# Optimization experiments

Hardware: AMD Instinct MI355X
Metric: run time of the kernel (lower is better)

The kernel has to match this reference:

```python
import jax, jax.numpy as jnp
import numpy as np

HEAD = 64            # RWKV_HEAD_SIZE
C = 1024             # n_embd = dim_att
F = 4096             # dim_ffn
B, T = 8, 256
H = C // HEAD
N_LAYER, LAYER_ID = 12, 1
GN_EPS = 1e-5 * 8 ** 2   # GroupNorm eps = 1e-5 * head_size_divisor^2


def bshift(x):
    """bidirectional_shift_multihead: per head, first half of channels shifted
    forward in time (right), second half shifted backward (left), zero-padded."""
    b, t, c = x.shape
    x4 = x.reshape(b, t, c // HEAD, HEAD)
    mid = HEAD // 2
    f = jnp.pad(x4[:, :-1, :, :mid], ((0, 0), (1, 0), (0, 0), (0, 0)))
    r = jnp.pad(x4[:, 1:, :, mid:], ((0, 0), (0, 1), (0, 0), (0, 0)))
    return jnp.concatenate([f, r], -1).reshape(b, t, c)


def layernorm(x, g, b):
    m = jnp.mean(x, -1, keepdims=True)
    v = jnp.mean((x - m) ** 2, -1, keepdims=True)
    return (x - m) * jax.lax.rsqrt(v + 1e-5) * g + b


def groupnorm(x, g, b):
    bb, t, c = x.shape
    xg = x.reshape(bb, t, H, HEAD)
    m = jnp.mean(xg, -1, keepdims=True)
    v = jnp.mean((xg - m) ** 2, -1, keepdims=True)
    return ((xg - m) * jax.lax.rsqrt(v + GN_EPS)).reshape(bb, t, c) * g + b


def wkv6_bi(r, k, v, w, u):
    """Bidirectional WKV6. r,k,v,w: [B,T,H,N]; u: [H,N].
    y_t = r_t . (S^fwd_t + u*k_t v_t^T + S^bwd_t), with per-channel decay
    d_t = exp(-exp(w_t)) applied to the state after each step in each direction."""
    d = jnp.exp(-jnp.exp(w))
    rT, kT, vT, dT = (jnp.moveaxis(a, 1, 0) for a in (r, k, v, d))  # [T,B,H,N]
    S0 = jnp.zeros((B, H, HEAD, HEAD), r.dtype)
    uB = u[None]  # [1,H,N]

    def fstep(S, inp):
        rt, kt, vt, dt = inp
        kv = kt[..., None] * vt[..., None, :]              # [B,H,N,N]
        y = jnp.einsum('bhj,bhji->bhi', rt, S + uB[..., None] * kv)
        return dt[..., None] * S + kv, y

    _, yf = jax.lax.scan(fstep, S0, (rT, kT, vT, dT))

    def bstep(S, inp):
        rt, kt, vt, dt = inp
        y = jnp.einsum('bhj,bhji->bhi', rt, S)
        return dt[..., None] * S + kt[..., None] * vt[..., None, :], y

    _, yb = jax.lax.scan(bstep, S0, (rT, kT, vT, dT), reverse=True)
    return jnp.moveaxis(yf + yb, 0, 1)  # [B,T,H,N]


def block_forward(x, ln1_g, ln1_b, ln2_g, ln2_b,
                  maa_x, maa_w, maa_k, maa_v, maa_r, maa_g, maa_w1, maa_w2,
                  time_decay, tdw1, tdw2, u, Wr, Wk, Wv, Wg, Wo, lnx_g, lnx_b,
                  cmaa_k, cmaa_r, Wck, Wcv, Wcr):
    # ---- RWKV_Tmix_V6 (attention) branch ----
    xa = layernorm(x, ln1_g, ln1_b)
    xx = bshift(xa) - xa
    a = jnp.tanh((xa + xx * maa_x) @ maa_w1).reshape(B, T, 5, -1)   # [B,T,5,32]
    m = jnp.einsum('btfd,fdc->fbtc', a, maa_w2)                      # [5,B,T,C]
    xw = xa + xx * (maa_w + m[0])
    xk = xa + xx * (maa_k + m[1])
    xv = xa + xx * (maa_v + m[2])
    xr = xa + xx * (maa_r + m[3])
    xg = xa + xx * (maa_g + m[4])
    r = (xr @ Wr).reshape(B, T, H, HEAD)
    k = (xk @ Wk).reshape(B, T, H, HEAD)
    v = (xv @ Wv).reshape(B, T, H, HEAD)
    g = jax.nn.silu(xg @ Wg)
    w = (time_decay + jnp.tanh(xw @ tdw1) @ tdw2).reshape(B, T, H, HEAD)
    y = wkv6_bi(r, k, v, w, u).reshape(B, T, C)
    y = groupnorm(y, lnx_g, lnx_b)
    x = x + (y * g) @ Wo
    # ---- RWKV_CMix_V6 (FFN) branch ----
    xc = layernorm(x, ln2_g, ln2_b)
    cxx = bshift(xc) - xc
    kk = jnp.square(jax.nn.relu((xc + cxx * cmaa_k) @ Wck))
    kv = kk @ Wcv
    x = x + jax.nn.sigmoid((xc + cxx * cmaa_r) @ Wcr) * kv
    return x


def setup_inputs() -> dict:
    key = jax.random.key(0)
    ks = jax.random.split(key, 16)
    r1 = 1.0 - LAYER_ID / N_LAYER            # ratio_1_to_almost0
    r0 = LAYER_ID / (N_LAYER - 1)            # ratio_0_to_1
    ddd = np.arange(C, dtype=np.float64) / C
    base = (1.0 - ddd ** r1).astype(np.float32)
    half = (1.0 - ddd ** (0.5 * r1)).astype(np.float32)
    s = 0.02
    p = {}
    p['x'] = jax.random.normal(ks[0], (B, T, C), jnp.float32)
    p['ln1_g'] = jnp.ones((C,), jnp.float32)
    p['ln1_b'] = jnp.zeros((C,), jnp.float32)
    p['ln2_g'] = jnp.ones((C,), jnp.float32)
    p['ln2_b'] = jnp.zeros((C,), jnp.float32)
    p['maa_x'] = jnp.asarray(base)
    p['maa_w'] = jnp.asarray(base)
    p['maa_k'] = jnp.asarray(base)
    p['maa_v'] = jnp.asarray((1.0 - (ddd ** r1 + 0.3 * r0)).astype(np.float32))
    p['maa_r'] = jnp.asarray(half)
    p['maa_g'] = jnp.asarray(half)
    p['maa_w1'] = jax.random.uniform(ks[1], (C, 160), jnp.float32, -0.01, 0.01)
    p['maa_w2'] = jax.random.uniform(ks[2], (5, 32, C), jnp.float32, -0.01, 0.01)
    n = np.arange(C, dtype=np.float64)
    p['time_decay'] = jnp.asarray((-6.0 + 5.0 * (n / (C - 1)) ** (0.7 + 1.3 * r0)).astype(np.float32))
    p['tdw1'] = jax.random.uniform(ks[3], (C, 64), jnp.float32, -0.01, 0.01)
    p['tdw2'] = jax.random.uniform(ks[4], (64, C), jnp.float32, -0.01, 0.01)
    faaaa = r0 * (1.0 - n / (C - 1)) + ((n + 1) % 3 - 1) * 0.1
    p['u'] = jnp.asarray(faaaa.reshape(H, HEAD).astype(np.float32))
    p['Wr'] = jax.random.normal(ks[5], (C, C), jnp.float32) * s
    p['Wk'] = jax.random.normal(ks[6], (C, C), jnp.float32) * s
    p['Wv'] = jax.random.normal(ks[7], (C, C), jnp.float32) * s
    p['Wg'] = jax.random.normal(ks[8], (C, C), jnp.float32) * s
    p['Wo'] = jax.random.normal(ks[9], (C, C), jnp.float32) * s
    p['lnx_g'] = jnp.ones((C,), jnp.float32)
    p['lnx_b'] = jnp.zeros((C,), jnp.float32)
    p['cmaa_k'] = jnp.asarray(base)
    p['cmaa_r'] = jnp.asarray(base)
    p['Wck'] = jax.random.normal(ks[10], (C, F), jnp.float32) * s
    p['Wcv'] = jax.random.normal(ks[11], (F, C), jnp.float32) * s
    p['Wcr'] = jax.random.normal(ks[12], (C, C), jnp.float32) * s
    return p


def reference(x, ln1_g, ln1_b, ln2_g, ln2_b,
              maa_x, maa_w, maa_k, maa_v, maa_r, maa_g, maa_w1, maa_w2,
              time_decay, tdw1, tdw2, u, Wr, Wk, Wv, Wg, Wo, lnx_g, lnx_b,
              cmaa_k, cmaa_r, Wck, Wcv, Wcr):
    return block_forward(x, ln1_g, ln1_b, ln2_g, ln2_b,
                         maa_x, maa_w, maa_k, maa_v, maa_r, maa_g, maa_w1, maa_w2,
                         time_decay, tdw1, tdw2, u, Wr, Wk, Wv, Wg, Wo, lnx_g, lnx_b,
                         cmaa_k, cmaa_r, Wck, Wcv, Wcr)
```

## Files before the change

kernel.cpp:

```cpp
#include <hip/hip_runtime.h>
#include <math.h>
#include <stdint.h>

static constexpr int B  = 8;
static constexpr int T  = 256;
static constexpr int C  = 1024;
static constexpr int H  = 16;
static constexpr int HEAD = 64;
static constexpr int FF = 4096;
static constexpr int BT = B * T;
static constexpr int NCH = 8;
static constexpr int CS  = 32;

typedef short short8  __attribute__((ext_vector_type(8)));
typedef float floatx4 __attribute__((ext_vector_type(4)));

__device__ __forceinline__ float bf2f(ushort u) {
    return __uint_as_float(((uint32_t)u) << 16);
}
__device__ __forceinline__ ushort f2bf(float x) {
    uint32_t u = __float_as_uint(x);
    u += 0x7fff + ((u >> 16) & 1);
    return (ushort)(u >> 16);
}

__device__ __forceinline__ void gload16(const void* g, void* l) {
    __builtin_amdgcn_global_load_lds(
        (const __attribute__((address_space(1))) unsigned int*)g,
        (__attribute__((address_space(3))) unsigned int*)l, 16, 0, 0);
}

#define BEPI_NONE_BF   0
#define BEPI_SILU_BF   1
#define BEPI_RELUSQ_BF 2
#define BEPI_NONE_F    3
#define BEPI_RES_F     4
#define BEPI_SIGRES_F  5
#define BEPI_TANH_F    6
#define BEPI_TANH_BF   7
#define BEPI_DECAY_F   8
#define BEPI_SIGRES2_F 9

__global__ __launch_bounds__(256) void ln_kernel(const float* __restrict__ x,
                                                 const float* __restrict__ g,
                                                 const float* __restrict__ b,
                                                 float* __restrict__ out)
{
    const int row = blockIdx.x;
    const int tid = threadIdx.x;
    const float4 v = reinterpret_cast<const float4*>(x + (size_t)row * C)[tid];
    float s = v.x + v.y + v.z + v.w;
#pragma unroll
    for (int off = 32; off > 0; off >>= 1) s += __shfl_xor(s, off);
    __shared__ float red[8];
    const int wave = tid >> 6, lane = tid & 63;
    if (lane == 0) red[wave] = s;
    __syncthreads();
    const float mean = (red[0] + red[1] + red[2] + red[3]) * (1.0f / C);
    const float d0 = v.x - mean, d1 = v.y - mean, d2 = v.z - mean, d3 = v.w - mean;
    float q = d0 * d0 + d1 * d1 + d2 * d2 + d3 * d3;
#pragma unroll
    for (int off = 32; off > 0; off >>= 1) q += __shfl_xor(q, off);
    if (lane == 0) red[4 + wave] = q;
    __syncthreads();
    const float var = (red[4] + red[5] + red[6] + red[7]) * (1.0f / C);
    const float rstd = rsqrtf(var + 1e-5f);
    const int c = tid * 4;
    float4 o;
    o.x = d0 * rstd * g[c + 0] + b[c + 0];
    o.y = d1 * rstd * g[c + 1] + b[c + 1];
    o.z = d2 * rstd * g[c + 2] + b[c + 2];
    o.w = d3 * rstd * g[c + 3] + b[c + 3];
    reinterpret_cast<float4*>(out + (size_t)row * C)[tid] = o;
}

__global__ __launch_bounds__(256) void bshiftmix_kernel(const float* __restrict__ xa,
                                                        const float* __restrict__ maa,
                                                        float* __restrict__ xx,
                                                        ushort* __restrict__ ax)
{
    const int i = blockIdx.x * 256 + threadIdx.x;
    const int c = i & (C - 1);
    const int bt = i >> 10;
    const int t = bt & (T - 1);
    const int j = c & (HEAD - 1);
    float src = 0.f;
    if (j < HEAD / 2) { if (t > 0)     src = xa[i - C]; }
    else              { if (t < T - 1) src = xa[i + C]; }
    const float a = xa[i];
    const float xv = src - a;
    xx[i] = xv;
    ax[i] = f2bf(a + xv * maa[c]);
}

__global__ __launch_bounds__(256) void bshiftcmix_kernel(const float* __restrict__ xc,
                                                         const float* __restrict__ mk,
                                                         const float* __restrict__ mr,
                                                         ushort* __restrict__ ok,
                                                         ushort* __restrict__ orr)
{
    const int i = blockIdx.x * 256 + threadIdx.x;
    const int c = i & (C - 1);
    const int bt = i >> 10;
    const int t = bt & (T - 1);
    const int j = c & (HEAD - 1);
    float src = 0.f;
    if (j < HEAD / 2) { if (t > 0)     src = xc[i - C]; }
    else              { if (t < T - 1) src = xc[i + C]; }
    const float a = xc[i];
    const float cxx = src - a;
    ok[i]  = f2bf(a + cxx * mk[c]);
    orr[i] = f2bf(a + cxx * mr[c]);
}

__global__ __launch_bounds__(1024) void gnmul_kernel(const float* __restrict__ yf,
                                                     const float* __restrict__ yb,
                                                     const float* __restrict__ g,
                                                     const float* __restrict__ b,
                                                     const ushort* __restrict__ gate,
                                                     const ushort* __restrict__ vin,
                                                     const ushort* __restrict__ rbuf,
                                                     const ushort* __restrict__ kbuf,
                                                     const float* __restrict__ u,
                                                     ushort* __restrict__ out)
{
    const int row = blockIdx.x;
    const int tid = threadIdx.x;
    const size_t idx = (size_t)row * C + tid;
    float p = bf2f(rbuf[idx]) * bf2f(kbuf[idx]) * u[tid];
#pragma unroll
    for (int off = 32; off > 0; off >>= 1) p += __shfl_xor(p, off);
    const float v = yf[idx] + yb[idx] + p * bf2f(vin[idx]);
    float s = v;
#pragma unroll
    for (int off = 32; off > 0; off >>= 1) s += __shfl_xor(s, off);
    const float m = s * (1.0f / HEAD);
    const float d = v - m;
    float q = d * d;
#pragma unroll
    for (int off = 32; off > 0; off >>= 1) q += __shfl_xor(q, off);
    const float rstd = rsqrtf(q * (1.0f / HEAD) + 6.4e-4f);
    out[idx] = f2bf((d * rstd * g[tid] + b[tid]) * bf2f(gate[idx]));
}

__global__ __launch_bounds__(256) void wconv_kernel(const float* __restrict__ W,
                                                    ushort* __restrict__ Wt,
                                                    int Kd, int Nd)
{
    __shared__ float tile[32][33];
    const int n0 = blockIdx.x * 32, k0 = blockIdx.y * 32;
    const int tx = threadIdx.x, ty = threadIdx.y;
#pragma unroll
    for (int i = 0; i < 4; ++i)
        tile[ty * 4 + i][tx] = W[(size_t)(k0 + ty * 4 + i) * Nd + n0 + tx];
    __syncthreads();
#pragma unroll
    for (int i = 0; i < 4; ++i)
        Wt[(size_t)(n0 + ty * 4 + i) * Kd + k0 + tx] = f2bf(tile[tx][ty * 4 + i]);
}

__global__ __launch_bounds__(256) void w2conv_kernel(const float* __restrict__ w2,
                                                     ushort* __restrict__ w2t)
{
    __shared__ float tile[32][33];
    const int f = blockIdx.y;
    const int n0 = blockIdx.x * 32;
    const int tx = threadIdx.x, ty = threadIdx.y;
#pragma unroll
    for (int i = 0; i < 4; ++i)
        tile[ty * 4 + i][tx] = w2[(size_t)f * 32 * C + (size_t)(ty * 4 + i) * C + n0 + tx];
    __syncthreads();
#pragma unroll
    for (int i = 0; i < 4; ++i)
        w2t[(size_t)f * C * 32 + (size_t)(n0 + ty * 4 + i) * 32 + tx] = f2bf(tile[tx][ty * 4 + i]);
}

struct Wconv4Args { const float* W[4]; };
__global__ __launch_bounds__(256) void wconv4_kernel(Wconv4Args args, ushort* __restrict__ Wt)
{
    __shared__ float tile[32][33];
    const int z = blockIdx.z;
    const float* __restrict__ W = args.W[z];
    ushort* __restrict__ dst = Wt + (size_t)z * C * C;
    const int n0 = blockIdx.x * 32, k0 = blockIdx.y * 32;
    const int tx = threadIdx.x, ty = threadIdx.y;
#pragma unroll
    for (int i = 0; i < 4; ++i)
        tile[ty * 4 + i][tx] = W[(size_t)(k0 + ty * 4 + i) * C + n0 + tx];
    __syncthreads();
#pragma unroll
    for (int i = 0; i < 4; ++i)
        dst[(size_t)(n0 + ty * 4 + i) * C + k0 + tx] = f2bf(tile[tx][ty * 4 + i]);
}

struct Mix5Args { const float* maa[5]; ushort* out[5]; };
__global__ __launch_bounds__(256) void mix5m_kernel(const ushort* __restrict__ a5b,
                                                    const ushort* __restrict__ w2t,
                                                    const float* __restrict__ xa,
                                                    const float* __restrict__ xx,
                                                    Mix5Args args)
{
    __shared__ __align__(16) ushort As[128 * 32];
    __shared__ __align__(16) ushort Bs[64 * 32];
    const int f = blockIdx.z;
    const int bm = blockIdx.y * 128, bn = blockIdx.x * 64;
    const int tid = threadIdx.x;
    const int wid = tid >> 6, lane = tid & 63;
    const int wr = wid >> 1, wc = wid & 1;
    const int l15 = lane & 15, lhi = lane >> 4;

#pragma unroll
    for (int p = 0; p < 2; ++p) {
        const int lin = p * 256 + tid;
        const int row = lin >> 2;
        const int sp = (lin & 3) ^ ((row >> 1) & 3);
        gload16(a5b + (size_t)(bm + row) * 160 + f * 32 + sp * 8, &As[lin * 8]);
    }
    {
        const int lin = tid;
        const int n = lin >> 2;
        const int sp = (lin & 3) ^ ((n >> 1) & 3);
        gload16(w2t + ((size_t)f * C + bn + n) * 32 + sp * 8, &Bs[lin * 8]);
    }
    __syncthreads();

    short8 af[4], bfr[2];
#pragma unroll
    for (int m = 0; m < 4; ++m) {
        const int row = wr * 64 + m * 16 + l15;
        const int sp = lhi ^ ((row >> 1) & 3);
        af[m] = *(const short8*)&As[row * 32 + sp * 8];
    }
#pragma unroll
    for (int n = 0; n < 2; ++n) {
        const int col = wc * 32 + n * 16 + l15;
        const int sp = lhi ^ ((col >> 1) & 3);
        bfr[n] = *(const short8*)&Bs[col * 32 + sp * 8];
    }
    floatx4 acc[4][2];
#pragma unroll
    for (int m = 0; m < 4; ++m)
#pragma unroll
        for (int n = 0; n < 2; ++n)
            acc[m][n] = __builtin_amdgcn_mfma_f32_16x16x32_bf16(
                af[m], bfr[n], (floatx4){0.f, 0.f, 0.f, 0.f}, 0, 0, 0);

    const float* __restrict__ maa = args.maa[f];
    ushort* __restrict__ out = args.out[f];
#pragma unroll
    for (int m = 0; m < 4; ++m) {
        const int row0 = bm + wr * 64 + m * 16 + lhi * 4;
#pragma unroll
        for (int n = 0; n < 2; ++n) {
            const int col = bn + wc * 32 + n * 16 + l15;
            const float mc = maa[col];
#pragma unroll
            for (int j = 0; j < 4; ++j) {
                const size_t oi = (size_t)(row0 + j) * C + col;
                out[oi] = f2bf(xa[oi] + xx[oi] * (mc + acc[m][n][j]));
            }
        }
    }
}

__global__ __launch_bounds__(256) void wkv_pass1(const ushort* __restrict__ k,
                                                 const ushort* __restrict__ v,
                                                 const float* __restrict__ d,
                                                 ushort* __restrict__ M,
                                                 float* __restrict__ D)
{
    const int uc = blockIdx.x;
    const int w = threadIdx.x >> 6, lane = threadIdx.x & 63;
    const int c = uc & (NCH - 1), unit = uc >> 3;
    const int dir = unit & 1, bh = unit >> 1;
    const int jb = w * 16;
    const size_t rowb = ((size_t)(bh >> 4) * T * H + (bh & 15)) * HEAD;
    __shared__ float Lk[4][CS][16], Ld[4][CS][16];

    const int s0 = c * CS;
    for (int idx = lane; idx < CS * 16; idx += 64) {
        const int s = idx >> 4, jj = idx & 15;
        const int t = dir ? (T - 1 - (s0 + s)) : (s0 + s);
        const size_t g = rowb + (size_t)t * (H * HEAD) + jb + jj;
        Lk[w][s][jj] = bf2f(k[g]);
        Ld[w][s][jj] = d[g];
    }
    float vr[CS];
#pragma unroll
    for (int s = 0; s < CS; ++s) {
        const int t = dir ? (T - 1 - (s0 + s)) : (s0 + s);
        vr[s] = bf2f(v[rowb + (size_t)t * (H * HEAD) + lane]);
    }
    __syncthreads();

    float S[16];
#pragma unroll
    for (int j = 0; j < 16; ++j) S[j] = 0.f;

    for (int ss = 0; ss < CS; ++ss) {
        const float vv = vr[ss];
        const float* __restrict__ sk = Lk[w][ss];
        const float* __restrict__ sd = Ld[w][ss];
#pragma unroll
        for (int jj = 0; jj < 16; jj += 4) {
            const float4 k4 = *reinterpret_cast<const float4*>(&sk[jj]);
            const float4 d4 = *reinterpret_cast<const float4*>(&sd[jj]);
            S[jj + 0] = fmaf(d4.x, S[jj + 0], k4.x * vv);
            S[jj + 1] = fmaf(d4.y, S[jj + 1], k4.y * vv);
            S[jj + 2] = fmaf(d4.z, S[jj + 2], k4.z * vv);
            S[jj + 3] = fmaf(d4.w, S[jj + 3], k4.w * vv);
        }
    }
    const size_t mb = (size_t)uc * 4096 + (size_t)lane * 64 + jb;
#pragma unroll
    for (int j = 0; j < 16; ++j) M[mb + j] = f2bf(S[j]);
    if (lane < 16) {
        float PD = 1.f;
#pragma unroll
        for (int s = 0; s < CS; ++s) PD *= Ld[w][s][lane];
        D[(size_t)uc * 64 + jb + lane] = PD;
    }
}

__global__ __launch_bounds__(1024) void wkv_pass2(ushort* __restrict__ M,
                                                  const float* __restrict__ D)
{
    const int unit = blockIdx.x;
    const int tid = threadIdx.x;
    const int j0 = (tid & 15) * 4;
    float S0 = 0.f, S1 = 0.f, S2 = 0.f, S3 = 0.f;
#pragma unroll
    for (int c = 0; c < NCH; ++c) {
        const int uc = unit * NCH + c;
        const float4 Dv = *reinterpret_cast<const float4*>(D + (size_t)uc * 64 + j0);
        ushort* mp = M + (size_t)uc * 4096 + tid * 4;
        const uint2 mv = *reinterpret_cast<const uint2*>(mp);
        const float m0 = bf2f((ushort)(mv.x & 0xffff));
        const float m1 = bf2f((ushort)(mv.x >> 16));
        const float m2 = bf2f((ushort)(mv.y & 0xffff));
        const float m3 = bf2f((ushort)(mv.y >> 16));
        uint2 sv;
        sv.x = (uint32_t)f2bf(S0) | ((uint32_t)f2bf(S1) << 16);
        sv.y = (uint32_t)f2bf(S2) | ((uint32_t)f2bf(S3) << 16);
        *reinterpret_cast<uint2*>(mp) = sv;
        S0 = fmaf(Dv.x, S0, m0);
        S1 = fmaf(Dv.y, S1, m1);
        S2 = fmaf(Dv.z, S2, m2);
        S3 = fmaf(Dv.w, S3, m3);
    }
}

__global__ __launch_bounds__(256) void wkv_ymfma(const ushort* __restrict__ r,
                                                 const ushort* __restrict__ k,
                                                 const ushort* __restrict__ v,
                                                 const float* __restrict__ d,
                                                 const ushort* __restrict__ Sin,
                                                 float* __restrict__ yf,
                                                 float* __restrict__ yb)
{
    const int uc = blockIdx.x;
    const int c = uc & (NCH - 1), unit = uc >> 3;
    const int dir = unit & 1, bh = unit >> 1;
    const int tid = threadIdx.x;
    const int wv = tid >> 6, lane = tid & 63;
    const int l15 = lane & 15, lhi = lane >> 4;
    const size_t rowb = ((size_t)(bh >> 4) * T * H + (bh & 15)) * HEAD;
    const int s0 = c * CS;

    __shared__ ushort rp[32][64];
    __shared__ ushort kp[32][64];
    __shared__ ushort vt[64][40];
    __shared__ ushort Pl[32][32];

    for (int idx = tid; idx < 32 * 64; idx += 256) {
        const int s = idx >> 6, j = idx & 63;
        const int t = dir ? (T - 1 - (s0 + s)) : (s0 + s);
        const size_t g = rowb + (size_t)t * (H * HEAD) + j;
        const int cs = (j >> 3) ^ (s & 7);
        rp[s][cs * 8 + (j & 7)] = r[g];
        kp[s][cs * 8 + (j & 7)] = k[g];
        vt[j][s] = v[g];
    }
    __syncthreads();

    if (tid < 64) {
        const int j = tid;
        float Q = 1.f, iQ = 1.f;
        for (int s = 0; s < 32; ++s) {
            const int t = dir ? (T - 1 - (s0 + s)) : (s0 + s);
            const float dd = d[rowb + (size_t)t * (H * HEAD) + j];
            const int a = ((j >> 3) ^ (s & 7)) * 8 + (j & 7);
            rp[s][a] = f2bf(bf2f(rp[s][a]) * Q);
            Q *= dd;
            iQ *= (1.0f / dd);
            kp[s][a] = f2bf(bf2f(kp[s][a]) * iQ);
        }
    }
    __syncthreads();

    const int st = wv & 1;
    const int ip = wv >> 1;

    short8 ar[2];
#pragma unroll
    for (int ks = 0; ks < 2; ++ks) {
        const int row = st * 16 + l15;
        const int ch = (ks * 4 + lhi) ^ (row & 7);
        ar[ks] = *(const short8*)&rp[row][ch * 8];
    }

    floatx4 acc[2];
#pragma unroll
    for (int n = 0; n < 2; ++n) {
        const int i = ip * 32 + n * 16 + l15;
        const ushort* sp = Sin + (size_t)uc * 4096 + (size_t)i * 64;
        const short8 b0 = *(const short8*)&sp[lhi * 8];
        const short8 b1 = *(const short8*)&sp[32 + lhi * 8];
        acc[n] = __builtin_amdgcn_mfma_f32_16x16x32_bf16(ar[0], b0, (floatx4){0.f, 0.f, 0.f, 0.f}, 0, 0, 0);
        acc[n] = __builtin_amdgcn_mfma_f32_16x16x32_bf16(ar[1], b1, acc[n], 0, 0, 0);
    }

    if (wv < 2) {
#pragma unroll
        for (int ut = 0; ut < 2; ++ut) {
            const int urow = ut * 16 + l15;
            const short8 bk0 = *(const short8*)&kp[urow][((0 + lhi) ^ (urow & 7)) * 8];
            const short8 bk1 = *(const short8*)&kp[urow][((4 + lhi) ^ (urow & 7)) * 8];
            floatx4 pa = __builtin_amdgcn_mfma_f32_16x16x32_bf16(ar[0], bk0, (floatx4){0.f, 0.f, 0.f, 0.f}, 0, 0, 0);
            pa = __builtin_amdgcn_mfma_f32_16x16x32_bf16(ar[1], bk1, pa, 0, 0, 0);
            const int sg0 = st * 16 + lhi * 4;
            const int ug = ut * 16 + l15;
#pragma unroll
            for (int jr = 0; jr < 4; ++jr) {
                const float val = (ug < sg0 + jr) ? pa[jr] : 0.f;
                Pl[sg0 + jr][ug] = f2bf(val);
            }
        }
    }
    __syncthreads();

    short8 ap;
    {
        const int row = st * 16 + l15;
        ap = *(const short8*)&Pl[row][lhi * 8];
    }
#pragma unroll
    for (int n = 0; n < 2; ++n) {
        const int i = ip * 32 + n * 16 + l15;
        const short8 bv = *(const short8*)&vt[i][lhi * 8];
        acc[n] = __builtin_amdgcn_mfma_f32_16x16x32_bf16(ap, bv, acc[n], 0, 0, 0);
    }

    float* __restrict__ yo = dir ? yb : yf;
#pragma unroll
    for (int n = 0; n < 2; ++n) {
        const int i = ip * 32 + n * 16 + l15;
#pragma unroll
        for (int jr = 0; jr < 4; ++jr) {
            const int sg = st * 16 + lhi * 4 + jr;
            const int t = dir ? (T - 1 - (s0 + sg)) : (s0 + sg);
            yo[rowb + (size_t)t * (H * HEAD) + i] = acc[n][jr];
        }
    }
}

template <int BN>
struct GemmLds {
    ushort As[2][128 * 64];
    ushort Bs[2][BN * 64];
};

template <int BN>
__device__ __forceinline__ void gemm_body(const ushort* __restrict__ A,
                                          const ushort* __restrict__ Bt,
                                          int bm, int bn, int K, int lda, int ldb,
                                          GemmLds<BN>& lds,
                                          floatx4 (&acc)[4][BN / 32])
{
    constexpr int NF = BN / 32;
    const int tid = threadIdx.x;
    const int wid = tid >> 6, lane = tid & 63;
    const int wr = wid >> 1, wc = wid & 1;
    const int l15 = lane & 15, lhi = lane >> 4;
    const int NT = K >> 6;

    auto stage = [&](int buf, int k0) {
#pragma unroll
        for (int p = 0; p < 4; ++p) {
            const int lin = p * 256 + tid;
            const int row = lin >> 3;
            const int cs = (lin & 7) ^ (row & 7);
            gload16(A + (size_t)(bm + row) * lda + k0 + cs * 8, &lds.As[buf][lin * 8]);
        }
#pragma unroll
        for (int p = 0; p < NF; ++p) {
            const int lin = p * 256 + tid;
            const int n = lin >> 3;
            const int cs = (lin & 7) ^ (n & 7);
            gload16(Bt + (size_t)(bn + n) * ldb + k0 + cs * 8, &lds.Bs[buf][lin * 8]);
        }
    };

    stage(0, 0);
    __syncthreads();
    for (int t = 0; t < NT; ++t) {
        const int cur = t & 1;
        if (t + 1 < NT) stage(cur ^ 1, (t + 1) << 6);

        short8 af[4][2];
#pragma unroll
        for (int m = 0; m < 4; ++m) {
            const int row = wr * 64 + m * 16 + l15;
#pragma unroll
            for (int s = 0; s < 2; ++s) {
                const int cc = (s * 4 + lhi) ^ (row & 7);
                af[m][s] = *(const short8*)&lds.As[cur][row * 64 + cc * 8];
            }
        }
        short8 bf[NF][2];
#pragma unroll
        for (int n = 0; n < NF; ++n) {
            const int col = wc * (BN / 2) + n * 16 + l15;
#pragma unroll
            for (int s = 0; s < 2; ++s) {
                const int cc = (s * 4 + lhi) ^ (col & 7);
                bf[n][s] = *(const short8*)&lds.Bs[cur][col * 64 + cc * 8];
            }
        }
#pragma unroll
        for (int m = 0; m < 4; ++m)
#pragma unroll
            for (int n = 0; n < NF; ++n) {
                acc[m][n] = __builtin_amdgcn_mfma_f32_16x16x32_bf16(af[m][0], bf[n][0], acc[m][n], 0, 0, 0);
                acc[m][n] = __builtin_amdgcn_mfma_f32_16x16x32_bf16(af[m][1], bf[n][1], acc[m][n], 0, 0, 0);
            }
        __syncthreads();
    }
}

template <int BN, int EPI>
__global__ __launch_bounds__(256) void bgemm_kernel(const ushort* __restrict__ A,
                                                    const ushort* __restrict__ Bt,
                                                    void* __restrict__ Cm,
                                                    int M, int N, int K,
                                                    const float* __restrict__ aux1,
                                                    const float* __restrict__ aux2,
                                                    const float* __restrict__ aux3)
{
    constexpr int NF = BN / 32;
    __shared__ GemmLds<BN> lds;
    int w = blockIdx.y * gridDim.x + blockIdx.x;
    const int nwg = gridDim.x * gridDim.y;
    if ((nwg & 7) == 0) w = (w & 7) * (nwg >> 3) + (w >> 3);
    const int bn = (w % gridDim.x) * BN;
    const int bm = (w / gridDim.x) * 128;
    const int tid = threadIdx.x;
    const int wid = tid >> 6, lane = tid & 63;
    const int wr = wid >> 1, wc = wid & 1;
    const int l15 = lane & 15, lhi = lane >> 4;

    floatx4 acc[4][NF];
#pragma unroll
    for (int m = 0; m < 4; ++m)
#pragma unroll
        for (int n = 0; n < NF; ++n) acc[m][n] = (floatx4){0.f, 0.f, 0.f, 0.f};

    gemm_body<BN>(A, Bt, bm, bn, K, K, K, lds, acc);

#pragma unroll
    for (int m = 0; m < 4; ++m) {
        const int row0 = bm + wr * 64 + m * 16 + lhi * 4;
#pragma unroll
        for (int n = 0; n < NF; ++n) {
            const int col = bn + wc * (BN / 2) + n * 16 + l15;
            if (col >= N) continue;
#pragma unroll
            for (int j = 0; j < 4; ++j) {
                const size_t oi = (size_t)(row0 + j) * N + col;
                const float a = acc[m][n][j];
                if constexpr (EPI == BEPI_NONE_BF) {
                    ((ushort*)Cm)[oi] = f2bf(a);
                } else if constexpr (EPI == BEPI_SILU_BF) {
                    ((ushort*)Cm)[oi] = f2bf(a / (1.f + __expf(-a)));
                } else if constexpr (EPI == BEPI_RELUSQ_BF) {
                    const float t = fmaxf(a, 0.f);
                    ((ushort*)Cm)[oi] = f2bf(t * t);
                } else if constexpr (EPI == BEPI_NONE_F) {
                    ((float*)Cm)[oi] = a;
                } else if constexpr (EPI == BEPI_RES_F) {
                    ((float*)Cm)[oi] = aux1[oi] + a;
                } else if constexpr (EPI == BEPI_SIGRES_F) {
                    ((float*)Cm)[oi] = aux1[oi] + aux2[oi] / (1.f + __expf(-a));
                } else if constexpr (EPI == BEPI_SIGRES2_F) {
                    ((float*)Cm)[oi] = aux1[oi] + (aux2[oi] + aux3[oi]) / (1.f + __expf(-a));
                } else if constexpr (EPI == BEPI_TANH_F) {
                    ((float*)Cm)[oi] = tanhf(a);
                } else if constexpr (EPI == BEPI_TANH_BF) {
                    ((ushort*)Cm)[oi] = f2bf(tanhf(a));
                } else {
                    ((float*)Cm)[oi] = __expf(-__expf(a + aux1[col]));
                }
            }
        }
    }
}

__global__ __launch_bounds__(256) void wcv_kernel(const ushort* __restrict__ A,
                                                  const ushort* __restrict__ Bt,
                                                  float* __restrict__ P0,
                                                  float* __restrict__ P1)
{
    __shared__ GemmLds<64> lds;
    const int z = blockIdx.z;
    int w = blockIdx.y * gridDim.x + blockIdx.x;
    w = (w & 7) * 32 + (w >> 3);
    const int bn = (w % 16) * 64;
    const int bm = (w / 16) * 128;
    const int tid = threadIdx.x;
    const int wid = tid >> 6, lane = tid & 63;
    const int wr = wid >> 1, wc = wid & 1;
    const int l15 = lane & 15, lhi = lane >> 4;

    floatx4 acc[4][2];
#pragma unroll
    for (int m = 0; m < 4; ++m)
#pragma unroll
        for (int n = 0; n < 2; ++n) acc[m][n] = (floatx4){0.f, 0.f, 0.f, 0.f};

    gemm_body<64>(A + z * (FF / 2), Bt + z * (FF / 2), bm, bn, FF / 2, FF, FF, lds, acc);

    float* __restrict__ P = z ? P1 : P0;
#pragma unroll
    for (int m = 0; m < 4; ++m) {
        const int row0 = bm + wr * 64 + m * 16 + lhi * 4;
#pragma unroll
        for (int n = 0; n < 2; ++n) {
            const int col = bn + wc * 32 + n * 16 + l15;
#pragma unroll
            for (int j = 0; j < 4; ++j)
                P[(size_t)(row0 + j) * C + col] = acc[m][n][j];
        }
    }
}

struct QkvgArgs { const ushort* A[4]; ushort* O[4]; };
__global__ __launch_bounds__(256) void qkvg_kernel(QkvgArgs args,
                                                   const ushort* __restrict__ Wt)
{
    __shared__ GemmLds<128> lds;
    const int z = blockIdx.z;
    int w = blockIdx.y * gridDim.x + blockIdx.x;
    w = (w & 7) * 16 + (w >> 3);
    const int bn = (w & 7) * 128;
    const int bm = (w >> 3) * 128;
    const int tid = threadIdx.x;
    const int wid = tid >> 6, lane = tid & 63;
    const int wr = wid >> 1, wc = wid & 1;
    const int l15 = lane & 15, lhi = lane >> 4;

    floatx4 acc[4][4];
#pragma unroll
    for (int m = 0; m < 4; ++m)
#pragma unroll
        for (int n = 0; n < 4; ++n) acc[m][n] = (floatx4){0.f, 0.f, 0.f, 0.f};

    gemm_body<128>(args.A[z], Wt + (size_t)z * C * C, bm, bn, C, C, C, lds, acc);

    ushort* __restrict__ O = args.O[z];
    const bool silu = (z == 3);
#pragma unroll
    for (int m = 0; m < 4; ++m) {
        const int row0 = bm + wr * 64 + m * 16 + lhi * 4;
#pragma unroll
        for (int n = 0; n < 4; ++n) {
            const int col = bn + wc * 64 + n * 16 + l15;
#pragma unroll
            for (int j = 0; j < 4; ++j) {
                float a = acc[m][n][j];
                if (silu) a = a / (1.f + __expf(-a));
                O[(size_t)(row0 + j) * C + col] = f2bf(a);
            }
        }
    }
}

extern "C" void kernel_launch(void* const* d_in, const int* in_sizes, int n_in,
                              void* d_out, int out_size, void* d_ws, size_t ws_size,
                              hipStream_t stream)
{
    const float* x        = (const float*)d_in[0];
    const float* ln1_g    = (const float*)d_in[1];
    const float* ln1_b    = (const float*)d_in[2];
    const float* ln2_g    = (const float*)d_in[3];
    const float* ln2_b    = (const float*)d_in[4];
    const float* maa_x    = (const float*)d_in[5];
    const float* maa_w    = (const float*)d_in[6];
    const float* maa_k    = (const float*)d_in[7];
    const float* maa_v    = (const float*)d_in[8];
    const float* maa_r    = (const float*)d_in[9];
    const float* maa_g    = (const float*)d_in[10];
    const float* maa_w1   = (const float*)d_in[11];
    const float* maa_w2   = (const float*)d_in[12];
    const float* time_dec = (const float*)d_in[13];
    const float* tdw1     = (const float*)d_in[14];
    const float* tdw2     = (const float*)d_in[15];
    const float* u        = (const float*)d_in[16];
    const float* Wr       = (const float*)d_in[17];
    const float* Wk       = (const float*)d_in[18];
    const float* Wv       = (const float*)d_in[19];
    const float* Wg       = (const float*)d_in[20];
    const float* Wo       = (const float*)d_in[21];
    const float* lnx_g    = (const float*)d_in[22];
    const float* lnx_b    = (const float*)d_in[23];
    const float* cmaa_k   = (const float*)d_in[24];
    const float* cmaa_r   = (const float*)d_in[25];
    const float* Wck      = (const float*)d_in[26];
    const float* Wcv      = (const float*)d_in[27];
    const float* Wcr      = (const float*)d_in[28];
    float* out = (float*)d_out;

    float* fws = (float*)d_ws;
    const size_t E = (size_t)BT * C;
    float* xa  = fws + 0 * E;
    float* xx  = fws + 1 * E;
    float* wd  = fws + 2 * E;
    float* fs  = fws + 3 * E;
    ushort* wBuf = (ushort*)(fws + 4 * E);
    ushort* Mbuf = (ushort*)fs;
    ushort* w2t  = wBuf + (size_t)C * 160;
    ushort* bf1  = wBuf + (size_t)C * FF;
    ushort* rb   = bf1 + E;
    ushort* kb   = rb + E;
    ushort* vb   = kb + E;
    ushort* gb   = vb + E;
    ushort* t1b  = gb + E;
    float* a5    = (float*)(t1b + (size_t)BT * 64);
    float* sig   = a5 + (size_t)BT * 160;
    float* Dbuf  = sig + (size_t)BT * H;
    ushort* a5b  = (ushort*)a5;
    ushort* xvb  = (ushort*)fs;
    ushort* xrb  = (ushort*)fs + E;
    ushort* xgb  = (ushort*)out;
    ushort* xwb  = (ushort*)out + E;
    ushort* kk   = (ushort*)xa;

    const dim3 blk(256);
    const dim3 tblk(32, 8);
    const int EW = (BT * C) / 256;
    const dim3 gNN(C / 64, BT / 128);

    ln_kernel<<<BT, blk, 0, stream>>>(x, ln1_g, ln1_b, xa);
    bshiftmix_kernel<<<EW, blk, 0, stream>>>(xa, maa_x, xx, bf1);
    wconv_kernel<<<dim3(160 / 32, C / 32), tblk, 0, stream>>>(maa_w1, wBuf, C, 160);
    bgemm_kernel<64, BEPI_TANH_BF><<<dim3(3, BT / 128), blk, 0, stream>>>(bf1, wBuf, a5b, BT, 160, C, nullptr, nullptr, nullptr);

    w2conv_kernel<<<dim3(C / 32, 5), tblk, 0, stream>>>(maa_w2, w2t);

    Mix5Args margs;
    margs.maa[0] = maa_w; margs.maa[1] = maa_k; margs.maa[2] = maa_v;
    margs.maa[3] = maa_r; margs.maa[4] = maa_g;
    margs.out[0] = xwb; margs.out[1] = bf1; margs.out[2] = xvb;
    margs.out[3] = xrb; margs.out[4] = xgb;
    mix5m_kernel<<<dim3(C / 64, BT / 128, 5), blk, 0, stream>>>(a5b, w2t, xa, xx, margs);

    wconv_kernel<<<dim3(64 / 32, C / 32), tblk, 0, stream>>>(tdw1, wBuf, C, 64);
    bgemm_kernel<64, BEPI_TANH_BF><<<dim3(1, BT / 128), blk, 0, stream>>>(xwb, wBuf, t1b, BT, 64, C, nullptr, nullptr, nullptr);
    wconv_kernel<<<dim3(C / 32, 64 / 32), tblk, 0, stream>>>(tdw2, wBuf, 64, C);
    bgemm_kernel<64, BEPI_DECAY_F><<<gNN, blk, 0, stream>>>(t1b, wBuf, wd, BT, C, 64, time_dec, nullptr, nullptr);

    Wconv4Args wargs;
    wargs.W[0] = Wk; wargs.W[1] = Wv; wargs.W[2] = Wr; wargs.W[3] = Wg;
    wconv4_kernel<<<dim3(C / 32, C / 32, 4), tblk, 0, stream>>>(wargs, wBuf);
    QkvgArgs qargs;
    qargs.A[0] = bf1; qargs.A[1] = xvb; qargs.A[2] = xrb; qargs.A[3] = xgb;
    qargs.O[0] = kb;  qargs.O[1] = vb;  qargs.O[2] = rb;  qargs.O[3] = gb;
    qkvg_kernel<<<dim3(8, 16, 4), blk, 0, stream>>>(qargs, wBuf);

    wkv_pass1<<<dim3(2 * B * H * NCH), blk, 0, stream>>>(kb, vb, wd, Mbuf, Dbuf);
    wkv_pass2<<<dim3(2 * B * H), dim3(1024), 0, stream>>>(Mbuf, Dbuf);
    wkv_ymfma<<<dim3(2 * B * H * NCH), blk, 0, stream>>>(rb, kb, vb, wd, Mbuf, xa, xx);

    gnmul_kernel<<<BT, dim3(1024), 0, stream>>>(xa, xx, lnx_g, lnx_b, gb, vb, rb, kb, u, vb);
    wconv_kernel<<<dim3(C / 32, C / 32), tblk, 0, stream>>>(Wo, wBuf, C, C);
    bgemm_kernel<64, BEPI_RES_F><<<gNN, blk, 0, stream>>>(vb, wBuf, out, BT, C, C, x, nullptr, nullptr);

    ln_kernel<<<BT, blk, 0, stream>>>(out, ln2_g, ln2_b, wd);
    bshiftcmix_kernel<<<EW, blk, 0, stream>>>(wd, cmaa_k, cmaa_r, bf1, gb);
    wconv_kernel<<<dim3(FF / 32, C / 32), tblk, 0, stream>>>(Wck, wBuf, C, FF);
    bgemm_kernel<128, BEPI_RELUSQ_BF><<<dim3(FF / 128, BT / 128), blk, 0, stream>>>(bf1, wBuf, kk, BT, FF, C, nullptr, nullptr, nullptr);
    wconv_kernel<<<dim3(C / 32, FF / 32), tblk, 0, stream>>>(Wcv, wBuf, FF, C);
    wcv_kernel<<<dim3(16, 16, 2), blk, 0, stream>>>(kk, wBuf, fs, wd);
    wconv_kernel<<<dim3(C / 32, C / 32), tblk, 0, stream>>>(Wcr, wBuf, C, C);
    bgemm_kernel<64, BEPI_SIGRES2_F><<<gNN, blk, 0, stream>>>(gb, wBuf, out, BT, C, C, out, fs, wd);

    (void)in_sizes; (void)n_in; (void)out_size; (void)ws_size;
}
```

Before: 268.5 us.

## Compute WKV chunk state with MFMA and split decay prefix across waves

Pass1 no longer runs a per-thread scalar recurrence over the chunk. It pre-scales k by the suffix product of decays and computes the chunk state as a single 64x64x32 bf16 matrix product on MFMA, with transposed k and v staged in shared memory. Pass3 now stages the decay values in shared memory so they are loaded coalesced, and splits the sequential r-scaling and k-inverse-scaling loops across two waves so they run in parallel. The bf16 rounding of the scaled k adds precision risk compared with the fp32 recurrence.

```diff
diff --git a/kernel.cpp b/kernel.cpp
--- a/kernel.cpp
+++ b/kernel.cpp
@@ -270,55 +270,52 @@
                                                  float* __restrict__ D)
 {
     const int uc = blockIdx.x;
-    const int w = threadIdx.x >> 6, lane = threadIdx.x & 63;
     const int c = uc & (NCH - 1), unit = uc >> 3;
     const int dir = unit & 1, bh = unit >> 1;
-    const int jb = w * 16;
+    const int tid = threadIdx.x;
+    const int wv = tid >> 6, lane = tid & 63;
+    const int l15 = lane & 15, lhi = lane >> 4;
     const size_t rowb = ((size_t)(bh >> 4) * T * H + (bh & 15)) * HEAD;
-    __shared__ float Lk[4][CS][16], Ld[4][CS][16];
-
     const int s0 = c * CS;
-    for (int idx = lane; idx < CS * 16; idx += 64) {
-        const int s = idx >> 4, jj = idx & 15;
+
+    __shared__ ushort kT[64][40];
+    __shared__ ushort vt[64][40];
+    __shared__ float  Ldd[CS][64];
+
+    for (int idx = tid; idx < CS * 64; idx += 256) {
+        const int s = idx >> 6, j = idx & 63;
         const int t = dir ? (T - 1 - (s0 + s)) : (s0 + s);
-        const size_t g = rowb + (size_t)t * (H * HEAD) + jb + jj;
-        Lk[w][s][jj] = bf2f(k[g]);
-        Ld[w][s][jj] = d[g];
-    }
-    float vr[CS];
-#pragma unroll
-    for (int s = 0; s < CS; ++s) {
-        const int t = dir ? (T - 1 - (s0 + s)) : (s0 + s);
-        vr[s] = bf2f(v[rowb + (size_t)t * (H * HEAD) + lane]);
-    }
-    __syncthreads();
-
-    float S[16];
-#pragma unroll
-    for (int j = 0; j < 16; ++j) S[j] = 0.f;
-
-    for (int ss = 0; ss < CS; ++ss) {
-        const float vv = vr[ss];
-        const float* __restrict__ sk = Lk[w][ss];
-        const float* __restrict__ sd = Ld[w][ss];
-#pragma unroll
-        for (int jj = 0; jj < 16; jj += 4) {
-            const float4 k4 = *reinterpret_cast<const float4*>(&sk[jj]);
-            const float4 d4 = *reinterpret_cast<const float4*>(&sd[jj]);
-            S[jj + 0] = fmaf(d4.x, S[jj + 0], k4.x * vv);
-            S[jj + 1] = fmaf(d4.y, S[jj + 1], k4.y * vv);
-            S[jj + 2] = fmaf(d4.z, S[jj + 2], k4.z * vv);
-            S[jj + 3] = fmaf(d4.w, S[jj + 3], k4.w * vv);
-        }
-    }
-    const size_t mb = (size_t)uc * 4096 + (size_t)lane * 64 + jb;
-#pragma unroll
-    for (int j = 0; j < 16; ++j) M[mb + j] = f2bf(S[j]);
-    if (lane < 16) {
-        float PD = 1.f;
-#pragma unroll
-        for (int s = 0; s < CS; ++s) PD *= Ld[w][s][lane];
-        D[(size_t)uc * 64 + jb + lane] = PD;
+        const size_t g = rowb + (size_t)t * (H * HEAD) + j;
+        kT[j][s] = k[g];
+        vt[j][s] = v[g];
+        Ldd[s][j] = d[g];
+    }
+    __syncthreads();
+
+    if (tid < 64) {
+        const int j = tid;
+        float G = 1.f;
+#pragma unroll
+        for (int s = CS - 1; s >= 0; --s) {
+            kT[j][s] = f2bf(bf2f(kT[j][s]) * G);
+            G *= Ldd[s][j];
+        }
+        D[(size_t)uc * 64 + j] = G;
+    }
+    __syncthreads();
+
+    const short8 av = *(const short8*)&vt[wv * 16 + l15][lhi * 8];
+    ushort* __restrict__ mrow = M + (size_t)uc * 4096;
+#pragma unroll
+    for (int n = 0; n < 4; ++n) {
+        const short8 bk = *(const short8*)&kT[n * 16 + l15][lhi * 8];
+        const floatx4 acc = __builtin_amdgcn_mfma_f32_16x16x32_bf16(
+            av, bk, (floatx4){0.f, 0.f, 0.f, 0.f}, 0, 0, 0);
+#pragma unroll
+        for (int jr = 0; jr < 4; ++jr) {
+            const int i = wv * 16 + lhi * 4 + jr;
+            mrow[(size_t)i * 64 + n * 16 + l15] = f2bf(acc[jr]);
+        }
     }
 }
 
@@ -371,6 +368,7 @@
     __shared__ ushort kp[32][64];
     __shared__ ushort vt[64][40];
     __shared__ ushort Pl[32][32];
+    __shared__ float  Ldd[CS][64];
 
     for (int idx = tid; idx < 32 * 64; idx += 256) {
         const int s = idx >> 6, j = idx & 63;
@@ -380,19 +378,26 @@
         rp[s][cs * 8 + (j & 7)] = r[g];
         kp[s][cs * 8 + (j & 7)] = k[g];
         vt[j][s] = v[g];
-    }
-    __syncthreads();
-
-    if (tid < 64) {
-        const int j = tid;
-        float Q = 1.f, iQ = 1.f;
+        Ldd[s][j] = d[g];
+    }
+    __syncthreads();
+
+    if (wv == 0) {
+        const int j = lane;
+        float Q = 1.f;
+#pragma unroll
         for (int s = 0; s < 32; ++s) {
-            const int t = dir ? (T - 1 - (s0 + s)) : (s0 + s);
-            const float dd = d[rowb + (size_t)t * (H * HEAD) + j];
             const int a = ((j >> 3) ^ (s & 7)) * 8 + (j & 7);
             rp[s][a] = f2bf(bf2f(rp[s][a]) * Q);
-            Q *= dd;
-            iQ *= (1.0f / dd);
+            Q *= Ldd[s][j];
+        }
+    } else if (wv == 1) {
+        const int j = lane;
+        float iQ = 1.f;
+#pragma unroll
+        for (int s = 0; s < 32; ++s) {
+            iQ *= (1.0f / Ldd[s][j]);
+            const int a = ((j >> 3) ^ (s & 7)) * 8 + (j & 7);
             kp[s][a] = f2bf(bf2f(kp[s][a]) * iQ);
         }
     }
```

After: 255.6 us. 4.8% less time.
